# Performance work log

Hardware: AMD Instinct MI355X
Metric: run time of the kernel (lower is better)

Reference implementation:

```python
import jax, jax.numpy as jnp
import numpy as np

HIDDEN = 2048
NH = 32       # num query heads
NKV = 8       # num kv heads
D = 64        # head_dim = hidden // NH
BSX, BSY = 32, 32  # block sizes


def setup_inputs() -> dict:
    key = jax.random.key(0)
    ks = jax.random.split(key, 5)
    B, L = 2, 4096  # L = x_dim * y_dim
    w = lambda k, sh, fan: jax.random.normal(k, sh, jnp.float32) * (fan ** -0.5)
    return {
        "hidden_states": jax.random.normal(ks[0], (B, L, HIDDEN), jnp.float32),
        "Wq": w(ks[1], (HIDDEN, NH * D), HIDDEN),
        "Wk": w(ks[2], (HIDDEN, NKV * D), HIDDEN),
        "Wv": w(ks[3], (HIDDEN, NKV * D), HIDDEN),
        "Wo": w(ks[4], (NH * D, HIDDEN), NH * D),
        "x_dim": 64,
        "y_dim": 64,
    }


def _block_split(x, B, bnx, bny, h):
    # einops: 'b (bnx bsx bny bsy) (h d) -> (b bnx bny) (bsx bsy) h d'
    x = x.reshape(B, bnx, BSX, bny, BSY, h, D)
    x = x.transpose(0, 1, 3, 2, 4, 5, 6)  # b bnx bny bsx bsy h d
    return x.reshape(B * bnx * bny, BSX * BSY, h, D)


def reference(hidden_states, Wq, Wk, Wv, Wo, x_dim, y_dim):
    B, L, _ = hidden_states.shape
    bnx, bny = x_dim // BSX, y_dim // BSY
    q = _block_split(hidden_states @ Wq, B, bnx, bny, NH)   # [nb, T, NH, D]
    k = _block_split(hidden_states @ Wk, B, bnx, bny, NKV)  # [nb, T, NKV, D]
    v = _block_split(hidden_states @ Wv, B, bnx, bny, NKV)
    g = NH // NKV  # GQA groups: query head i attends kv head i // g
    k = jnp.repeat(k, g, axis=2)
    v = jnp.repeat(v, g, axis=2)
    scores = jnp.einsum('nqhd,nkhd->nhqk', q, k) * (D ** -0.5)
    p = jax.nn.softmax(scores, axis=-1)
    o = jnp.einsum('nhqk,nkhd->nqhd', p, v)  # [nb, T, NH, D]
    # Faithful to the torch code: plain reshape (does NOT invert the block rearrange)
    o = o.reshape(B, L, NH * D)
    return o @ Wo
```

## Files before the change

kernel.cpp:

```cpp
#include <hip/hip_runtime.h>

typedef __bf16 bf16_t;
typedef __bf16 bf16x8 __attribute__((ext_vector_type(8)));
typedef __bf16 bf16x4 __attribute__((ext_vector_type(4)));
typedef float f32x4 __attribute__((ext_vector_type(4)));
typedef float f32x16 __attribute__((ext_vector_type(16)));
typedef short s16x4 __attribute__((ext_vector_type(4)));
typedef short s16x8 __attribute__((ext_vector_type(8)));
typedef unsigned u32x2 __attribute__((ext_vector_type(2)));

#define MFMA16(A_, B_, C_) __builtin_amdgcn_mfma_f32_16x16x32_bf16((A_), (B_), (C_), 0, 0, 0)
#define MFMA32(A_, B_, C_) __builtin_amdgcn_mfma_f32_32x32x16_bf16((A_), (B_), (C_), 0, 0, 0)

#define QSC 0.18033688011112042f

#if __has_builtin(__builtin_amdgcn_exp2f)
#define EXP2F(x) __builtin_amdgcn_exp2f(x)
#else
#define EXP2F(x) exp2f(x)
#endif

__device__ __forceinline__ void gload_lds16(const bf16_t* g, bf16_t* l) {
  __builtin_amdgcn_global_load_lds(
      (const __attribute__((address_space(1))) void*)g,
      (__attribute__((address_space(3))) void*)l, 16, 0, 0);
}

__device__ __forceinline__ unsigned cvt_pk_bf16(float a, float b) {
  unsigned r;
  asm("v_cvt_pk_bf16_f32 %0, %1, %2" : "=v"(r) : "v"(a), "v"(b));
  return r;
}

__device__ __forceinline__ s16x4 tr_b16(const bf16_t* p) {
  s16x4 d;
  unsigned off = (unsigned)(size_t)(const __attribute__((address_space(3))) bf16_t*)p;
  asm volatile("ds_read_b64_tr_b16 %0, %1" : "=v"(d) : "v"(off));
  return d;
}

union B128 { s16x8 s; bf16x8 b; };

#define DSR(PTR, U)                                                           \
  do {                                                                        \
    unsigned _o = (unsigned)(size_t)                                          \
        (const __attribute__((address_space(3))) bf16_t*)(PTR);               \
    asm volatile("ds_read_b128 %0, %1" : "=v"((U).s) : "v"(_o));              \
  } while (0)

#define DSR_OFS(BASEV, OFFSTR, U)                                             \
  asm volatile("ds_read_b128 %0, %1 offset:" OFFSTR                           \
               : "=v"((U).s) : "v"(BASEV))

__device__ __forceinline__ void swap32(unsigned a, unsigned b, int hi,
                                       unsigned& ra, unsigned& rb) {
#if __has_builtin(__builtin_amdgcn_permlane32_swap)
  u32x2 r = __builtin_amdgcn_permlane32_swap(b, a, false, false);
  rb = r[0]; ra = r[1];
#else
  unsigned bx = (unsigned)__shfl_xor((int)b, 32);
  unsigned ax = (unsigned)__shfl_xor((int)a, 32);
  ra = hi ? a : bx;
  rb = hi ? ax : b;
#endif
}

__global__ __launch_bounds__(256) void k_convert(const float* __restrict__ in,
                                                 bf16_t* __restrict__ out, int n4) {
  int i = blockIdx.x * 256 + threadIdx.x;
  if (i >= n4) return;
  float4 v = ((const float4*)in)[i];
  bf16x4 o;
  o[0] = (__bf16)v.x; o[1] = (__bf16)v.y; o[2] = (__bf16)v.z; o[3] = (__bf16)v.w;
  *(bf16x4*)(out + (size_t)i * 4) = o;
}

__global__ __launch_bounds__(256) void k_transpose(const float* __restrict__ in,
                                                   bf16_t* __restrict__ out, int R, int C) {
  __shared__ float tile[64][65];
  int tx = threadIdx.x & 63;
  int ty = threadIdx.x >> 6;
  int bc = blockIdx.x * 64;
  int br = blockIdx.y * 64;
#pragma unroll
  for (int i = ty; i < 64; i += 4)
    tile[i][tx] = in[(size_t)(br + i) * C + bc + tx];
  __syncthreads();
#pragma unroll
  for (int i = ty; i < 64; i += 4)
    out[(size_t)(bc + i) * R + br + tx] = (bf16_t)tile[tx][i];
}

__device__ __forceinline__ int permrow(int r) {
  int b  = r >> 12;
  int l  = r & 4095;
  int ix = (l >> 11) & 1;
  int sx = (l >> 6) & 31;
  int iy = (l >> 5) & 1;
  int sy = l & 31;
  return (b << 12) + (ix << 11) + (iy << 10) + (sx << 5) + sy;
}

#define SBAR __builtin_amdgcn_sched_barrier(0)

#define LA(K_) (lds + (K_)*24576)
#define LB(K_) (lds + (K_)*24576 + 16384)

template <int MODE>
__global__ __launch_bounds__(512, 2) void k_gemm15(
    const bf16_t* __restrict__ A,
    const bf16_t* __restrict__ B0, const bf16_t* __restrict__ B1,
    const bf16_t* __restrict__ B2,
    bf16_t* __restrict__ Cq, bf16_t* __restrict__ Ck, bf16_t* __restrict__ Cv,
    float* __restrict__ Cf) {
  extern __shared__ bf16_t lds[];

  const int TN = (MODE == 0) ? 24 : 16;
  int bid = blockIdx.x;
  int s = bid >> 3;
  int tm = (bid & 7) * 4 + s / TN;
  int tn = s % TN;

  const bf16_t* Bp;
  int brow;
  if (MODE == 0) {
    if (tn < 16)      { Bp = B0; brow = tn << 7; }
    else if (tn < 20) { Bp = B1; brow = (tn - 16) << 7; }
    else              { Bp = B2; brow = (tn - 20) << 7; }
  } else {
    Bp = B0; brow = tn << 7;
  }

  int tid = threadIdx.x;
  int lane = tid & 63;
  int w = tid >> 6;
  int wm = w >> 1, wn = w & 1;
  int g16 = lane >> 4, cl = lane & 15;
  int swz8 = (cl & 7) << 3;
  int wofs = w << 9;

  int srow = tid >> 3;
  int lc = (((tid & 7) ^ (srow & 7)) << 3);
  const bf16_t* aBt = A + (size_t)(tm * 256 + srow) * 2048 + lc;
  const bf16_t* bBt = Bp + (size_t)(brow + srow) * 2048 + lc;

  unsigned ldsb = (unsigned)(size_t)(__attribute__((address_space(3))) bf16_t*)lds;
  unsigned arow0 = (unsigned)((wm * 64 + cl) * 128 + (((g16 * 8) ^ swz8) << 1));
  unsigned arow1 = (unsigned)((wm * 64 + cl) * 128 + ((((32 + g16 * 8)) ^ swz8) << 1));
  unsigned brow0 = (unsigned)(32768 + (wn * 64 + cl) * 128 + (((g16 * 8) ^ swz8) << 1));
  unsigned brow1 = (unsigned)(32768 + (wn * 64 + cl) * 128 + ((((32 + g16 * 8)) ^ swz8) << 1));
  unsigned a0[3], a1[3], b0[3], b1[3];
#pragma unroll
  for (int kk = 0; kk < 3; ++kk) {
    a0[kk] = ldsb + kk * 49152 + arow0;
    a1[kk] = ldsb + kk * 49152 + arow1;
    b0[kk] = ldsb + kk * 49152 + brow0;
    b1[kk] = ldsb + kk * 49152 + brow1;
  }

#define GA_STAGE(K2_)                                                          \
  _Pragma("unroll") for (int rr = 0; rr < 4; ++rr)                             \
    gload_lds16(aBt + (size_t)(rr * 64) * 2048, LA(K2_) + rr * 4096 + wofs);   \
  _Pragma("unroll") for (int rr = 0; rr < 2; ++rr)                             \
    gload_lds16(bBt + (size_t)(rr * 64) * 2048, LB(K2_) + rr * 4096 + wofs);   \
  aBt += 64; bBt += 64;

#define GA_MFMA_M(M_)                                                          \
  _Pragma("unroll") for (int kk = 0; kk < 2; ++kk)                             \
    _Pragma("unroll") for (int ni = 0; ni < 4; ++ni)                           \
      acc[M_][ni] = MFMA16(af[M_][kk].b, bfr[ni][kk].b, acc[M_][ni]);

#define GA_BODY(K_, K2_, VMSTR_, DOSTAGE_)                                     \
  {                                                                            \
    B128 af[4][2], bfr[4][2];                                                  \
    asm volatile("s_waitcnt vmcnt(" VMSTR_ ")" ::: "memory");                  \
    __builtin_amdgcn_s_barrier();                                              \
    DSR_OFS(b0[K_], "0",    bfr[0][0]); DSR_OFS(b0[K_], "2048", bfr[1][0]);    \
    DSR_OFS(b0[K_], "4096", bfr[2][0]); DSR_OFS(b0[K_], "6144", bfr[3][0]);    \
    DSR_OFS(b1[K_], "0",    bfr[0][1]); DSR_OFS(b1[K_], "2048", bfr[1][1]);    \
    DSR_OFS(b1[K_], "4096", bfr[2][1]); DSR_OFS(b1[K_], "6144", bfr[3][1]);    \
    DSR_OFS(a0[K_], "0",    af[0][0]);  DSR_OFS(a1[K_], "0",    af[0][1]);     \
    DSR_OFS(a0[K_], "2048", af[1][0]);  DSR_OFS(a1[K_], "2048", af[1][1]);     \
    DSR_OFS(a0[K_], "4096", af[2][0]);  DSR_OFS(a1[K_], "4096", af[2][1]);     \
    DSR_OFS(a0[K_], "6144", af[3][0]);  DSR_OFS(a1[K_], "6144", af[3][1]);     \
    if (DOSTAGE_) { GA_STAGE(K2_); }                                           \
    asm volatile("s_waitcnt lgkmcnt(6)" ::: "memory");                         \
    SBAR;                                                                      \
    __builtin_amdgcn_s_setprio(1);                                             \
    GA_MFMA_M(0);                                                              \
    asm volatile("s_waitcnt lgkmcnt(4)" ::: "memory");                         \
    SBAR;                                                                      \
    GA_MFMA_M(1);                                                              \
    asm volatile("s_waitcnt lgkmcnt(2)" ::: "memory");                         \
    SBAR;                                                                      \
    GA_MFMA_M(2);                                                              \
    asm volatile("s_waitcnt lgkmcnt(0)" ::: "memory");                         \
    SBAR;                                                                      \
    GA_MFMA_M(3);                                                              \
    __builtin_amdgcn_s_setprio(0);                                             \
  }

  f32x4 acc[4][4];
#pragma unroll
  for (int i = 0; i < 4; ++i)
#pragma unroll
    for (int j = 0; j < 4; ++j) acc[i][j] = (f32x4)(0.0f);

  GA_STAGE(0);
  GA_STAGE(1);

  for (int t3 = 0; t3 < 30; t3 += 3) {
    GA_BODY(0, 2, "6", 1);
    GA_BODY(1, 0, "6", 1);
    GA_BODY(2, 1, "6", 1);
  }
  GA_BODY(0, 2, "6", 0);
  GA_BODY(1, 0, "0", 0);

#pragma unroll
  for (int mi = 0; mi < 4; ++mi) {
#pragma unroll
    for (int rr = 0; rr < 4; ++rr) {
      int r = tm * 256 + wm * 64 + mi * 16 + g16 * 4 + rr;
      if (MODE == 0) {
        int rp = permrow(r);
#pragma unroll
        for (int ni = 0; ni < 4; ++ni) {
          int c = tn * 128 + wn * 64 + ni * 16 + cl;
          float v = acc[mi][ni][rr];
          if (c < 2048)      Cq[(size_t)rp * 2048 + c] = (bf16_t)(v * QSC);
          else if (c < 2560) Ck[(size_t)rp * 512 + (c - 2048)] = (bf16_t)v;
          else               Cv[(size_t)rp * 512 + (c - 2560)] = (bf16_t)v;
        }
      } else {
#pragma unroll
        for (int ni = 0; ni < 4; ++ni) {
          int c = tn * 128 + wn * 64 + ni * 16 + cl;
          Cf[(size_t)r * 2048 + c] = acc[mi][ni][rr];
        }
      }
    }
  }
}

__global__ __launch_bounds__(256, 2) void k_attn(
    const bf16_t* __restrict__ Qp, const bf16_t* __restrict__ Kp,
    const bf16_t* __restrict__ Vp, bf16_t* __restrict__ O) {
  int bid = blockIdx.x;
  int qc = bid & 7;
  int h  = (bid >> 3) & 31;
  int n  = bid >> 8;
  int kvh = h >> 2;

  __shared__ bf16_t buf[2][8192];

  int tid = threadIdx.x, lane = tid & 63, w = tid >> 6;
  int l31 = lane & 31, hi = lane >> 5;
  int qrow_blk = n * 1024 + qc * 128;
  bf16_t* base = &buf[0][0];

#pragma unroll
  for (int r = 0; r < 4; ++r) {
    int ql = r * 32 + (tid >> 3);
    int cs = (tid & 7) << 4;
    int lc = (cs ^ ((ql & 7) << 4)) >> 1;
    gload_lds16(Qp + (size_t)(qrow_blk + ql) * 2048 + h * 64 + lc,
                base + r * 2048 + w * 512);
  }
  __syncthreads();
  bf16x8 qf[4];
  {
    int q = w * 32 + l31;
    const bf16_t* qrow = base + q * 64;
    int sw = (q & 7) << 4;
#pragma unroll
    for (int c = 0; c < 4; ++c)
      qf[c] = *(const bf16x8*)(qrow + (((c * 32 + hi * 16) ^ sw) >> 1));
  }
  __syncthreads();

  f32x16 oacc0 = (f32x16)(0.0f), oacc1 = (f32x16)(0.0f);
  float m_run = -1e30f, l_run = 0.0f;

  auto stageKV = [&](int t) {
    bf16_t* bp = &buf[t & 1][0];
    int kvb = n * 1024 + t * 64;
#pragma unroll
    for (int r = 0; r < 2; ++r) {
      int kv = r * 32 + (tid >> 3);
      int cs = (tid & 7) << 4;
      int lc = (cs ^ ((kv & 7) << 4)) >> 1;
      gload_lds16(Kp + (size_t)(kvb + kv) * 512 + kvh * 64 + lc,
                  bp + r * 2048 + w * 512);
    }
#pragma unroll
    for (int r = 0; r < 2; ++r) {
      int slot = r * 256 + tid;
      int sub = slot >> 3;
      int kb = sub >> 2, db = sub & 3;
      int j = (slot >> 1) & 3, hf = slot & 1;
      gload_lds16(Vp + (size_t)(kvb + kb * 4 + j) * 512 + kvh * 64 + db * 16 + hf * 8,
                  bp + 4096 + r * 2048 + w * 512);
    }
  };

  stageKV(0);
  for (int t = 0; t < 16; ++t) {
    __syncthreads();
    if (t < 15) stageKV(t + 1);
    const bf16_t* bp = &buf[t & 1][0];
    const bf16_t* Vs = bp + 4096;

#pragma unroll
    for (int s = 0; s < 2; ++s) {
      f32x16 st = (f32x16)(0.0f);
      {
        int kv = s * 32 + l31;
        const bf16_t* krow = bp + kv * 64;
        int sw = (kv & 7) << 4;
#pragma unroll
        for (int c = 0; c < 4; ++c) {
          bf16x8 kf = *(const bf16x8*)(krow + (((c * 32 + hi * 16) ^ sw) >> 1));
          st = MFMA32(kf, qf[c], st);
        }
      }
      float p0 = fmaxf(fmaxf(st[0], st[1]), st[2]);
      float p1 = fmaxf(fmaxf(st[3], st[4]), st[5]);
      float p2 = fmaxf(fmaxf(st[6], st[7]), st[8]);
      float p3 = fmaxf(fmaxf(st[9], st[10]), st[11]);
      float p4 = fmaxf(fmaxf(st[12], st[13]), st[14]);
      float pmax = fmaxf(fmaxf(fmaxf(p0, p1), p2),
                         fmaxf(fmaxf(p3, p4), st[15]));
      pmax = fmaxf(pmax, __shfl_xor(pmax, 32));
      if (!__all(pmax <= m_run + 11.0f)) {
        float mnew = fmaxf(m_run, pmax);
        float resc = EXP2F(m_run - mnew);
        l_run *= resc;
#pragma unroll
        for (int e = 0; e < 16; ++e) { oacc0[e] *= resc; oacc1[e] *= resc; }
        m_run = mnew;
      }
      float rs = 0.0f;
      unsigned pw[8];
#pragma unroll
      for (int u = 0; u < 8; ++u) {
        float q0 = EXP2F(st[2 * u] - m_run);
        float q1 = EXP2F(st[2 * u + 1] - m_run);
        rs += q0 + q1;
        pw[u] = cvt_pk_bf16(q0, q1);
      }
      rs += __shfl_xor(rs, 32);
      l_run += rs;

#pragma unroll
      for (int c = 0; c < 2; ++c) {
        unsigned w2, w0, w3, w1;
        swap32(pw[c * 4 + 2], pw[c * 4 + 0], hi, w2, w0);
        swap32(pw[c * 4 + 3], pw[c * 4 + 1], hi, w3, w1);
        union { unsigned u[4]; bf16x8 v; } pa;
        pa.u[0] = w0; pa.u[1] = w1; pa.u[2] = w2; pa.u[3] = w3;
        int kb0 = s * 8 + c * 4 + hi * 2;
        int dbl = l31 >> 4;
        int cc8 = (l31 & 15) * 4;
        const bf16_t* p00 = Vs + (kb0 * 4 + dbl) * 64 + cc8;
        const bf16_t* p01 = Vs + ((kb0 + 1) * 4 + dbl) * 64 + cc8;
        const bf16_t* p10 = Vs + (kb0 * 4 + 2 + dbl) * 64 + cc8;
        const bf16_t* p11 = Vs + ((kb0 + 1) * 4 + 2 + dbl) * 64 + cc8;
        s16x4 t00 = tr_b16(p00), t01 = tr_b16(p01);
        s16x4 t10 = tr_b16(p10), t11 = tr_b16(p11);
        asm volatile("s_waitcnt lgkmcnt(0)" ::: "memory");
        __builtin_amdgcn_sched_barrier(0);
        union { s16x4 s4[2]; bf16x8 v; } vf0, vf1;
        vf0.s4[0] = t00; vf0.s4[1] = t01;
        vf1.s4[0] = t10; vf1.s4[1] = t11;
        oacc0 = MFMA32(pa.v, vf0.v, oacc0);
        oacc1 = MFMA32(pa.v, vf1.v, oacc1);
      }
    }
  }

  float linv = 1.0f / l_run;
#pragma unroll
  for (int r = 0; r < 16; ++r) {
    int qrw = (r & 3) + 8 * (r >> 2) + 4 * hi;
    float li = __shfl(linv, qrw);
    size_t orow = (size_t)(qrow_blk + w * 32 + qrw) * 2048 + h * 64 + l31;
    O[orow]      = (bf16_t)(oacc0[r] * li);
    O[orow + 32] = (bf16_t)(oacc1[r] * li);
  }
}

extern "C" void kernel_launch(void* const* d_in, const int* in_sizes, int n_in,
                              void* d_out, int out_size, void* d_ws, size_t ws_size,
                              hipStream_t stream) {
  const float* X  = (const float*)d_in[0];
  const float* Wq = (const float*)d_in[1];
  const float* Wk = (const float*)d_in[2];
  const float* Wv = (const float*)d_in[3];
  const float* Wo = (const float*)d_in[4];
  float* out = (float*)d_out;

  char* ws = (char*)d_ws;
  const size_t MB = 1024 * 1024;
  bf16_t* Xb  = (bf16_t*)(ws + 0);
  bf16_t* WqT = (bf16_t*)(ws + 32 * MB);
  bf16_t* WkT = (bf16_t*)(ws + 40 * MB);
  bf16_t* WvT = (bf16_t*)(ws + 42 * MB);
  bf16_t* WoT = (bf16_t*)(ws + 44 * MB);
  bf16_t* Qp  = (bf16_t*)(ws + 52 * MB);
  bf16_t* Kp  = (bf16_t*)(ws + 84 * MB);
  bf16_t* Vp  = (bf16_t*)(ws + 92 * MB);
  bf16_t* Ob  = (bf16_t*)(ws + 100 * MB);

  hipFuncSetAttribute(reinterpret_cast<const void*>(&k_gemm15<0>),
                      hipFuncAttributeMaxDynamicSharedMemorySize, 147456);
  hipFuncSetAttribute(reinterpret_cast<const void*>(&k_gemm15<1>),
                      hipFuncAttributeMaxDynamicSharedMemorySize, 147456);

  k_convert<<<16384, 256, 0, stream>>>(X, Xb, 4194304);
  k_transpose<<<dim3(32, 32), 256, 0, stream>>>(Wq, WqT, 2048, 2048);
  k_transpose<<<dim3(8, 32), 256, 0, stream>>>(Wk, WkT, 2048, 512);
  k_transpose<<<dim3(8, 32), 256, 0, stream>>>(Wv, WvT, 2048, 512);
  k_transpose<<<dim3(32, 32), 256, 0, stream>>>(Wo, WoT, 2048, 2048);

  k_gemm15<0><<<768, 512, 147456, stream>>>(Xb, WqT, WkT, WvT, Qp, Kp, Vp,
                                            nullptr);
  k_attn<<<2048, 256, 0, stream>>>(Qp, Kp, Vp, Ob);
  k_gemm15<1><<<512, 512, 147456, stream>>>(Ob, WoT, nullptr, nullptr, nullptr,
                                            nullptr, nullptr, out);
}
```

Measured before the change: 321.3 us.

## Replace output projection GEMM with 256x256-tile double-buffered kernel

Adds a dedicated output-projection GEMM that uses 256x256 tiles (8 waves, each computing 128x64) with a two-stage LDS double buffer and swizzled rows, replacing the 128-wide generic kernel. Larger tiles cut global/LDS reloads per FLOP and halve the block count to 256, roughly one wave per CU on the device. The trade-offs are more accumulator registers per thread, fewer blocks (tail/occupancy risk), and a staggered lgkmcnt wait scheme that depends on exact LDS read ordering.

Result: no change. 325.4 us (+1.3%).

```diff
diff --git a/kernel.cpp b/kernel.cpp
--- a/kernel.cpp
+++ b/kernel.cpp
@@ -243,6 +243,120 @@
   }
 }
 
+__global__ __launch_bounds__(512, 2) void k_gemmB256(
+    const bf16_t* __restrict__ A, const bf16_t* __restrict__ B0,
+    float* __restrict__ Cf) {
+  extern __shared__ bf16_t lds[];
+
+  int bid = blockIdx.x;
+  int s = bid >> 3;
+  int tm = (bid & 7) * 4 + (s >> 3);
+  int tn = s & 7;
+
+  int tid = threadIdx.x;
+  int lane = tid & 63;
+  int w = tid >> 6;
+  int wm = w >> 2, wn = w & 3;
+  int g16 = lane >> 4, cl = lane & 15;
+  int swz8 = (cl & 7) << 3;
+  int wofs = w << 9;
+
+  int srow = tid >> 3;
+  int lc = (((tid & 7) ^ (srow & 7)) << 3);
+  const bf16_t* aBt = A + (size_t)(tm * 256 + srow) * 2048 + lc;
+  const bf16_t* bBt = B0 + (size_t)(tn * 256 + srow) * 2048 + lc;
+
+  unsigned ldsb = (unsigned)(size_t)(__attribute__((address_space(3))) bf16_t*)lds;
+  unsigned arow0 = (unsigned)((wm * 128 + cl) * 128 + (((g16 * 8) ^ swz8) << 1));
+  unsigned arow1 = (unsigned)((wm * 128 + cl) * 128 + ((((32 + g16 * 8)) ^ swz8) << 1));
+  unsigned brw0 = (unsigned)(32768 + (wn * 64 + cl) * 128 + (((g16 * 8) ^ swz8) << 1));
+  unsigned brw1 = (unsigned)(32768 + (wn * 64 + cl) * 128 + ((((32 + g16 * 8)) ^ swz8) << 1));
+  unsigned a0[2], a1[2], b0[2], b1[2];
+#pragma unroll
+  for (int kk = 0; kk < 2; ++kk) {
+    a0[kk] = ldsb + kk * 65536 + arow0;
+    a1[kk] = ldsb + kk * 65536 + arow1;
+    b0[kk] = ldsb + kk * 65536 + brw0;
+    b1[kk] = ldsb + kk * 65536 + brw1;
+  }
+
+#define GB_STAGE(K_)                                                           \
+  _Pragma("unroll") for (int rr = 0; rr < 4; ++rr)                             \
+    gload_lds16(aBt + (size_t)(rr * 64) * 2048,                                \
+                lds + (K_) * 32768 + rr * 4096 + wofs);                        \
+  _Pragma("unroll") for (int rr = 0; rr < 4; ++rr)                             \
+    gload_lds16(bBt + (size_t)(rr * 64) * 2048,                                \
+                lds + (K_) * 32768 + 16384 + rr * 4096 + wofs);                \
+  aBt += 64; bBt += 64;
+
+#define GB_MFMA_M(M_)                                                          \
+  _Pragma("unroll") for (int kk = 0; kk < 2; ++kk)                             \
+    _Pragma("unroll") for (int ni = 0; ni < 4; ++ni)                           \
+      acc[M_][ni] = MFMA16(af[M_][kk].b, bfr[ni][kk].b, acc[M_][ni]);
+
+#define GB_WAIT(N_) asm volatile("s_waitcnt lgkmcnt(" N_ ")" ::: "memory"); SBAR;
+
+#define GB_BODY(K_, VMSTR_, DOSTAGE_)                                          \
+  {                                                                            \
+    B128 af[8][2], bfr[4][2];                                                  \
+    asm volatile("s_waitcnt vmcnt(" VMSTR_ ")" ::: "memory");                  \
+    __builtin_amdgcn_s_barrier();                                              \
+    DSR_OFS(b0[K_], "0",    bfr[0][0]); DSR_OFS(b0[K_], "2048", bfr[1][0]);    \
+    DSR_OFS(b0[K_], "4096", bfr[2][0]); DSR_OFS(b0[K_], "6144", bfr[3][0]);    \
+    DSR_OFS(b1[K_], "0",    bfr[0][1]); DSR_OFS(b1[K_], "2048", bfr[1][1]);    \
+    DSR_OFS(b1[K_], "4096", bfr[2][1]); DSR_OFS(b1[K_], "6144", bfr[3][1]);    \
+    DSR_OFS(a0[K_], "0",     af[0][0]); DSR_OFS(a1[K_], "0",     af[0][1]);    \
+    DSR_OFS(a0[K_], "2048",  af[1][0]); DSR_OFS(a1[K_], "2048",  af[1][1]);    \
+    DSR_OFS(a0[K_], "4096",  af[2][0]); DSR_OFS(a1[K_], "4096",  af[2][1]);    \
+    DSR_OFS(a0[K_], "6144",  af[3][0]); DSR_OFS(a1[K_], "6144",  af[3][1]);    \
+    DSR_OFS(a0[K_], "8192",  af[4][0]); DSR_OFS(a1[K_], "8192",  af[4][1]);    \
+    DSR_OFS(a0[K_], "10240", af[5][0]); DSR_OFS(a1[K_], "10240", af[5][1]);    \
+    DSR_OFS(a0[K_], "12288", af[6][0]); DSR_OFS(a1[K_], "12288", af[6][1]);    \
+    DSR_OFS(a0[K_], "14336", af[7][0]); DSR_OFS(a1[K_], "14336", af[7][1]);    \
+    __builtin_amdgcn_s_setprio(1);                                             \
+    GB_WAIT("14"); GB_MFMA_M(0);                                               \
+    GB_WAIT("12"); GB_MFMA_M(1);                                               \
+    GB_WAIT("10"); GB_MFMA_M(2);                                               \
+    GB_WAIT("8");  GB_MFMA_M(3);                                               \
+    GB_WAIT("6");  GB_MFMA_M(4);                                               \
+    GB_WAIT("4");  GB_MFMA_M(5);                                               \
+    GB_WAIT("2");  GB_MFMA_M(6);                                               \
+    GB_WAIT("0");  GB_MFMA_M(7);                                               \
+    __builtin_amdgcn_s_setprio(0);                                             \
+    __builtin_amdgcn_s_barrier();                                              \
+    if (DOSTAGE_) { GB_STAGE(K_); }                                            \
+  }
+
+  f32x4 acc[8][4];
+#pragma unroll
+  for (int i = 0; i < 8; ++i)
+#pragma unroll
+    for (int j = 0; j < 4; ++j) acc[i][j] = (f32x4)(0.0f);
+
+  GB_STAGE(0);
+  GB_STAGE(1);
+
+  for (int t2 = 0; t2 < 15; ++t2) {
+    GB_BODY(0, "8", 1);
+    GB_BODY(1, "8", 1);
+  }
+  GB_BODY(0, "8", 0);
+  GB_BODY(1, "0", 0);
+
+#pragma unroll
+  for (int mi = 0; mi < 8; ++mi) {
+#pragma unroll
+    for (int rr = 0; rr < 4; ++rr) {
+      int r = tm * 256 + wm * 128 + mi * 16 + g16 * 4 + rr;
+#pragma unroll
+      for (int ni = 0; ni < 4; ++ni) {
+        int c = tn * 256 + wn * 64 + ni * 16 + cl;
+        Cf[(size_t)r * 2048 + c] = acc[mi][ni][rr];
+      }
+    }
+  }
+}
+
 __global__ __launch_bounds__(256, 2) void k_attn(
     const bf16_t* __restrict__ Qp, const bf16_t* __restrict__ Kp,
     const bf16_t* __restrict__ Vp, bf16_t* __restrict__ O) {
@@ -414,8 +528,8 @@
 
   hipFuncSetAttribute(reinterpret_cast<const void*>(&k_gemm15<0>),
                       hipFuncAttributeMaxDynamicSharedMemorySize, 147456);
-  hipFuncSetAttribute(reinterpret_cast<const void*>(&k_gemm15<1>),
-                      hipFuncAttributeMaxDynamicSharedMemorySize, 147456);
+  hipFuncSetAttribute(reinterpret_cast<const void*>(&k_gemmB256),
+                      hipFuncAttributeMaxDynamicSharedMemorySize, 131072);
 
   k_convert<<<16384, 256, 0, stream>>>(X, Xb, 4194304);
   k_transpose<<<dim3(32, 32), 256, 0, stream>>>(Wq, WqT, 2048, 2048);
@@ -426,6 +540,5 @@
   k_gemm15<0><<<768, 512, 147456, stream>>>(Xb, WqT, WkT, WvT, Qp, Kp, Vp,
                                             nullptr);
   k_attn<<<2048, 256, 0, stream>>>(Qp, Kp, Vp, Ob);
-  k_gemm15<1><<<512, 512, 147456, stream>>>(Ob, WoT, nullptr, nullptr, nullptr,
-                                            nullptr, nullptr, out);
-}
+  k_gemmB256<<<256, 512, 131072, stream>>>(Ob, WoT, out);
+}
```
